# Kernel tuning notes

Hardware: AMD Instinct MI355X
Metric: run time of the kernel (lower is better)

## Reference

```python
import jax, jax.numpy as jnp
import numpy as np

D_MODEL = 1024
NUM_HEADS = 16
DEPTH = D_MODEL // NUM_HEADS


def setup_inputs() -> dict:
    key = jax.random.key(0)
    ks = jax.random.split(key, 9)
    B, S = 2, 2048
    s = 1.0 / np.sqrt(D_MODEL)
    inp = {
        "inputs": jax.random.normal(ks[0], (B, S, D_MODEL), dtype=jnp.float32),
        "wq": jax.random.normal(ks[1], (D_MODEL, D_MODEL), dtype=jnp.float32) * s,
        "bq": jnp.zeros((D_MODEL,), dtype=jnp.float32),
        "wk": jax.random.normal(ks[2], (D_MODEL, D_MODEL), dtype=jnp.float32) * s,
        "bk": jnp.zeros((D_MODEL,), dtype=jnp.float32),
        "wv": jax.random.normal(ks[3], (D_MODEL, D_MODEL), dtype=jnp.float32) * s,
        "bv": jnp.zeros((D_MODEL,), dtype=jnp.float32),
        "wo": jax.random.normal(ks[4], (D_MODEL, D_MODEL), dtype=jnp.float32) * s,
        "bo": jnp.zeros((D_MODEL,), dtype=jnp.float32),
    }
    return inp


def _split_heads(x, B):
    # [B, S, D] -> [B, H, S, depth]
    S = x.shape[1]
    return x.reshape(B, S, NUM_HEADS, DEPTH).transpose(0, 2, 1, 3)


def reference(inputs, wq, bq, wk, bk, wv, bv, wo, bo):
    B, S, _ = inputs.shape
    q = _split_heads(inputs @ wq + bq, B)  # [B,H,S,d]
    k = _split_heads(inputs @ wk + bk, B)
    v = _split_heads(inputs @ wv + bv, B)
    scale = 1.0 / jnp.sqrt(jnp.asarray(DEPTH, dtype=inputs.dtype))
    logits = jnp.einsum("bhqd,bhkd->bhqk", q, k) * scale  # [B,H,S,S]
    attn = jax.nn.softmax(logits, axis=-1)
    out = jnp.einsum("bhqk,bhkd->bhqd", attn, v)  # [B,H,S,d]
    out = out.transpose(0, 2, 1, 3).reshape(B, S, D_MODEL)
    return out @ wo + bo
```

## Files before the change

kernel.cpp:

```cpp
#include <hip/hip_runtime.h>
#include <math.h>

#define SEQ     2048
#define DM      1024
#define NH      16
#define DEPTH   64
#define MTOT    4096

typedef __attribute__((ext_vector_type(8))) _Float16 f16x8;
typedef __attribute__((ext_vector_type(2))) __fp16   fp16v2;
typedef __attribute__((ext_vector_type(4))) float    f32x4;
typedef __attribute__((ext_vector_type(2))) unsigned u32x2;

static __device__ inline unsigned pkh(float a, float b) {
    union { fp16v2 h; unsigned u; } c;
    c.h = __builtin_amdgcn_cvt_pkrtz(a, b);
    return c.u;
}

#define GLOBAL_AS(p) ((const __attribute__((address_space(1))) void*)(p))
#define LDS_AS(p)    ((__attribute__((address_space(3))) void*)(p))

#define K2  0.18033688011112043f
#define C2 -17.31234049066756f
#define EXP2(x) __builtin_amdgcn_exp2f(x)

#define DMA_SRC_C8(lane)  ((((lane) & 3) ^ (((lane) >> 3) & 3)) * 8)
#define FRAG_C8(lx,quad)  ((((quad) ^ (((lx) >> 1) & 3))) * 8)
#define DMA_SRC64(lane)   ((((lane) & 7) ^ (((lane) >> 3) & 7)) * 8)
#define FRAG64(lx,c)      ((((c) ^ ((lx) & 7))) * 8)

__global__ __launch_bounds__(256)
void prep(const float* __restrict__ X,
          const float* __restrict__ w0, const float* __restrict__ w1,
          const float* __restrict__ w2, const float* __restrict__ w3,
          short* __restrict__ Xb,
          short* __restrict__ o0, short* __restrict__ o1,
          short* __restrict__ o2, short* __restrict__ o3) {
    const int t = threadIdx.x;
    const int z = blockIdx.z;
    if (z >= 4) {
        int r0 = (z - 4) * 1024 + blockIdx.x * 64;
        int c0 = blockIdx.y * 64;
        #pragma unroll
        for (int i = 0; i < 4; i++) {
            int row = r0 + i * 16 + (t >> 4);
            int c4  = c0 + (t & 15) * 4;
            float4 v = *(const float4*)&X[(size_t)row * DM + c4];
            u32x2 o; o.x = pkh(v.x, v.y); o.y = pkh(v.z, v.w);
            *(u32x2*)&Xb[(size_t)row * DM + c4] = o;
        }
        return;
    }
    const float* W; short* O;
    switch (z) {
        case 0: W = w0; O = o0; break;
        case 1: W = w1; O = o1; break;
        case 2: W = w2; O = o2; break;
        default: W = w3; O = o3; break;
    }
    __shared__ float Tf[64][65];
    const int k0 = blockIdx.x * 64, n0 = blockIdx.y * 64;
    #pragma unroll
    for (int i = 0; i < 4; i++) {
        int row = i * 16 + (t >> 4);
        int c4  = (t & 15) * 4;
        float4 v = *(const float4*)&W[(size_t)(k0 + row) * DM + n0 + c4];
        Tf[row][c4 + 0] = v.x; Tf[row][c4 + 1] = v.y;
        Tf[row][c4 + 2] = v.z; Tf[row][c4 + 3] = v.w;
    }
    __syncthreads();
    #pragma unroll
    for (int i = 0; i < 4; i++) {
        int nrow = i * 16 + (t >> 4);
        int kc4  = (t & 15) * 4;
        u32x2 o;
        o.x = pkh(Tf[kc4 + 0][nrow], Tf[kc4 + 1][nrow]);
        o.y = pkh(Tf[kc4 + 2][nrow], Tf[kc4 + 3][nrow]);
        *(u32x2*)&O[(size_t)(n0 + nrow) * DM + k0 + kc4] = o;
    }
}

__global__ __launch_bounds__(256)
void gemm_qkv(const short* __restrict__ Xb,
              const short* __restrict__ Wqt, const short* __restrict__ Wkt,
              const short* __restrict__ Wvt,
              const float* __restrict__ bq, const float* __restrict__ bk,
              const float* __restrict__ bv,
              short* __restrict__ Qw, short* __restrict__ Kw,
              short* __restrict__ Vtw) {
    const int z = blockIdx.z;
    const short* A; const short* B; const float* bias;
    if (z == 0)      { A = Xb;  B = Wqt; bias = bq; }
    else if (z == 1) { A = Xb;  B = Wkt; bias = bk; }
    else             { A = Wvt; B = Xb;  bias = bv; }
    const int bx = blockIdx.x;
    int m0, n0;
    if (z < 2) { n0 = (bx & 7) * 128; m0 = (bx >> 3) * 128; }
    else       { m0 = (bx & 7) * 128; n0 = (bx >> 3) * 128; }

    __shared__ short As[128 * 64];
    __shared__ short Bs[128 * 64];
    const int t = threadIdx.x, lane = t & 63, w = t >> 6;
    const int lx = lane & 15, quad = lane >> 4;
    const int wm = (w & 1) * 64, wn = (w >> 1) * 64;
    const int r8 = lane >> 3;
    const int cs = DMA_SRC64(lane);

    f32x4 acc[4][4];
    #pragma unroll
    for (int i = 0; i < 4; i++)
        #pragma unroll
        for (int j = 0; j < 4; j++)
            acc[i][j] = (f32x4){0.f, 0.f, 0.f, 0.f};

    for (int k0 = 0; k0 < DM; k0 += 64) {
        #pragma unroll
        for (int j = 0; j < 4; j++) {
            int rb = w * 32 + j * 8;
            __builtin_amdgcn_global_load_lds(
                GLOBAL_AS(A + (size_t)(m0 + rb + r8) * DM + k0 + cs),
                LDS_AS(As + rb * 64), 16, 0, 0);
            __builtin_amdgcn_global_load_lds(
                GLOBAL_AS(B + (size_t)(n0 + rb + r8) * DM + k0 + cs),
                LDS_AS(Bs + rb * 64), 16, 0, 0);
        }
        __syncthreads();

        #pragma unroll
        for (int ks = 0; ks < 2; ks++) {
            const int fo = FRAG64(lx, ks * 4 + quad);
            f16x8 af[4], bfr[4];
            #pragma unroll
            for (int mt = 0; mt < 4; mt++)
                af[mt] = *(f16x8*)&As[(wm + mt * 16 + lx) * 64 + fo];
            #pragma unroll
            for (int nt = 0; nt < 4; nt++)
                bfr[nt] = *(f16x8*)&Bs[(wn + nt * 16 + lx) * 64 + fo];
            #pragma unroll
            for (int mt = 0; mt < 4; mt++)
                #pragma unroll
                for (int nt = 0; nt < 4; nt++)
                    acc[mt][nt] = __builtin_amdgcn_mfma_f32_16x16x32_f16(
                        af[mt], bfr[nt], acc[mt][nt], 0, 0, 0);
        }
        __syncthreads();
    }

    if (z < 2) {
        short* Cp = (z == 0) ? Qw : Kw;
        float bi[4];
        #pragma unroll
        for (int nt = 0; nt < 4; nt++) bi[nt] = bias[n0 + wn + nt * 16 + lx];
        #pragma unroll
        for (int mt = 0; mt < 4; mt++) {
            #pragma unroll
            for (int reg = 0; reg < 4; reg++) {
                int row = m0 + wm + mt * 16 + quad * 4 + reg;
                u32x2 o;
                o.x = pkh(acc[mt][0][reg] + bi[0], acc[mt][1][reg] + bi[1]);
                o.y = pkh(acc[mt][2][reg] + bi[2], acc[mt][3][reg] + bi[3]);
                *(u32x2*)&Cp[(size_t)row * DM + n0 + wn + 4 * lx] = o;
            }
        }
    } else {
        int colbase = n0 + wn;
        int bsel    = colbase >> 11;
        int kb      = (colbase & 2047) & ~63;
        short* Vbh  = Vtw + (size_t)bsel * ((size_t)NH * DEPTH * SEQ);
        #pragma unroll
        for (int mt = 0; mt < 4; mt++) {
            #pragma unroll
            for (int reg = 0; reg < 4; reg++) {
                int row = m0 + wm + mt * 16 + quad * 4 + reg;
                float bb = bias[row];
                u32x2 o;
                o.x = pkh(acc[mt][0][reg] + bb, acc[mt][1][reg] + bb);
                o.y = pkh(acc[mt][2][reg] + bb, acc[mt][3][reg] + bb);
                *(u32x2*)&Vbh[(size_t)row * SEQ + kb + 4 * lx] = o;
            }
        }
    }
}

__global__ __launch_bounds__(256)
void gemm_out(const short* __restrict__ A, const short* __restrict__ B,
              const float* __restrict__ bias, float* __restrict__ C) {
    __shared__ short As[128 * 64];
    __shared__ short Bs[64 * 64];
    const int t = threadIdx.x, lane = t & 63, w = t >> 6;
    const int lx = lane & 15, quad = lane >> 4;
    const int n0 = blockIdx.x * 64, m0 = blockIdx.y * 128;
    const int wm = (w & 1) * 64, wn = (w >> 1) * 32;
    const int r8 = lane >> 3;
    const int cs = DMA_SRC64(lane);

    f32x4 acc[4][2];
    #pragma unroll
    for (int i = 0; i < 4; i++)
        #pragma unroll
        for (int j = 0; j < 2; j++)
            acc[i][j] = (f32x4){0.f, 0.f, 0.f, 0.f};

    for (int k0 = 0; k0 < DM; k0 += 64) {
        #pragma unroll
        for (int j = 0; j < 4; j++) {
            int rb = w * 32 + j * 8;
            __builtin_amdgcn_global_load_lds(
                GLOBAL_AS(A + (size_t)(m0 + rb + r8) * DM + k0 + cs),
                LDS_AS(As + rb * 64), 16, 0, 0);
        }
        #pragma unroll
        for (int j = 0; j < 2; j++) {
            int rb = w * 16 + j * 8;
            __builtin_amdgcn_global_load_lds(
                GLOBAL_AS(B + (size_t)(n0 + rb + r8) * DM + k0 + cs),
                LDS_AS(Bs + rb * 64), 16, 0, 0);
        }
        __syncthreads();

        #pragma unroll
        for (int ks = 0; ks < 2; ks++) {
            const int fo = FRAG64(lx, ks * 4 + quad);
            f16x8 af[4], bfr[2];
            #pragma unroll
            for (int mt = 0; mt < 4; mt++)
                af[mt] = *(f16x8*)&As[(wm + mt * 16 + lx) * 64 + fo];
            #pragma unroll
            for (int nt = 0; nt < 2; nt++)
                bfr[nt] = *(f16x8*)&Bs[(wn + nt * 16 + lx) * 64 + fo];
            #pragma unroll
            for (int mt = 0; mt < 4; mt++)
                #pragma unroll
                for (int nt = 0; nt < 2; nt++)
                    acc[mt][nt] = __builtin_amdgcn_mfma_f32_16x16x32_f16(
                        af[mt], bfr[nt], acc[mt][nt], 0, 0, 0);
        }
        __syncthreads();
    }

    #pragma unroll
    for (int mt = 0; mt < 4; mt++)
        #pragma unroll
        for (int nt = 0; nt < 2; nt++)
            #pragma unroll
            for (int reg = 0; reg < 4; reg++) {
                int row = m0 + wm + mt * 16 + quad * 4 + reg;
                int col = n0 + wn + nt * 16 + lx;
                C[(size_t)row * DM + col] = acc[mt][nt][reg] + bias[col];
            }
}

__global__ __launch_bounds__(256)
void flash_mfma(const short* __restrict__ Q, const short* __restrict__ K,
                const short* __restrict__ Vt, short* __restrict__ O) {
    __shared__ short Ks[2][2][64 * 32];
    __shared__ short Vs[2][2][64 * 32];
    __shared__ short Ps[128 * 72];

    const int t = threadIdx.x, lane = t & 63, w = t >> 6;
    const int lx = lane & 15, quad = lane >> 4;
    const int h = blockIdx.y, bb = blockIdx.z;
    const int q0 = blockIdx.x * 128;
    const int r4 = lane >> 2;
    const int cs  = DMA_SRC_C8(lane);
    const int fa  = FRAG_C8(lx, quad);

    f16x8 qa[2][2];
    #pragma unroll
    for (int mt = 0; mt < 2; mt++)
        #pragma unroll
        for (int ks = 0; ks < 2; ks++)
            qa[mt][ks] = *(const f16x8*)&Q[(size_t)(bb * SEQ + q0 + w * 32 + mt * 16 + lx) * DM
                                           + h * DEPTH + ks * 32 + quad * 8];

    f32x4 of[2][4];
    float l_acc[2][4];
    #pragma unroll
    for (int mt = 0; mt < 2; mt++) {
        #pragma unroll
        for (int dt = 0; dt < 4; dt++) of[mt][dt] = (f32x4){0.f, 0.f, 0.f, 0.f};
        #pragma unroll
        for (int reg = 0; reg < 4; reg++) l_acc[mt][reg] = 0.f;
    }

    const short* Kb = K  + (size_t)bb * SEQ * DM + h * DEPTH;
    const short* Vb = Vt + (size_t)(bb * NH + h) * DEPTH * SEQ;

    auto stage = [&](int kt, int sb) {
        const int kbase = kt * 64;
        const short* kg = Kb + (size_t)(kbase + w * 16 + r4) * DM;
        __builtin_amdgcn_global_load_lds(GLOBAL_AS(kg + cs),
                                         LDS_AS(&Ks[sb][0][w * 16 * 32]), 16, 0, 0);
        __builtin_amdgcn_global_load_lds(GLOBAL_AS(kg + 32 + cs),
                                         LDS_AS(&Ks[sb][1][w * 16 * 32]), 16, 0, 0);
        const short* vg = Vb + (size_t)(w * 16 + r4) * SEQ + kbase;
        __builtin_amdgcn_global_load_lds(GLOBAL_AS(vg + cs),
                                         LDS_AS(&Vs[sb][0][w * 16 * 32]), 16, 0, 0);
        __builtin_amdgcn_global_load_lds(GLOBAL_AS(vg + 32 + cs),
                                         LDS_AS(&Vs[sb][1][w * 16 * 32]), 16, 0, 0);
    };

    stage(0, 0);
    __syncthreads();

    int buf = 0;
    for (int kt = 0; kt < SEQ / 64; kt++) {
        if (kt + 1 < SEQ / 64) stage(kt + 1, buf ^ 1);

        f32x4 s[2][4];
        #pragma unroll
        for (int mt = 0; mt < 2; mt++)
            #pragma unroll
            for (int nt = 0; nt < 4; nt++)
                s[mt][nt] = (f32x4){0.f, 0.f, 0.f, 0.f};
        #pragma unroll
        for (int ks = 0; ks < 2; ks++) {
            f16x8 kb[4];
            #pragma unroll
            for (int nt = 0; nt < 4; nt++)
                kb[nt] = *(f16x8*)&Ks[buf][ks][(nt * 16 + lx) * 32 + fa];
            __builtin_amdgcn_s_setprio(1);
            #pragma unroll
            for (int mt = 0; mt < 2; mt++)
                #pragma unroll
                for (int nt = 0; nt < 4; nt++)
                    s[mt][nt] = __builtin_amdgcn_mfma_f32_16x16x32_f16(
                        qa[mt][ks], kb[nt], s[mt][nt], 0, 0, 0);
            __builtin_amdgcn_s_setprio(0);
        }

        #pragma unroll
        for (int mt = 0; mt < 2; mt++) {
            #pragma unroll
            for (int reg = 0; reg < 4; reg++) {
                float p0 = EXP2(fmaf(s[mt][0][reg], K2, C2));
                float p1 = EXP2(fmaf(s[mt][1][reg], K2, C2));
                float p2 = EXP2(fmaf(s[mt][2][reg], K2, C2));
                float p3 = EXP2(fmaf(s[mt][3][reg], K2, C2));
                l_acc[mt][reg] += (p0 + p1) + (p2 + p3);
                int rowoff = (w * 32 + mt * 16 + quad * 4 + reg) * 72;
                u32x2 pk; pk.x = pkh(p0, p1); pk.y = pkh(p2, p3);
                *(u32x2*)&Ps[rowoff + 4 * lx] = pk;
            }
        }

        #pragma unroll
        for (int ks = 0; ks < 2; ks++) {
            f16x8 vb[4], pa[2];
            #pragma unroll
            for (int dt = 0; dt < 4; dt++)
                vb[dt] = *(f16x8*)&Vs[buf][ks][(dt * 16 + lx) * 32 + fa];
            #pragma unroll
            for (int mt = 0; mt < 2; mt++)
                pa[mt] = *(f16x8*)&Ps[(w * 32 + mt * 16 + lx) * 72 + ks * 32 + quad * 8];
            __builtin_amdgcn_s_setprio(1);
            #pragma unroll
            for (int mt = 0; mt < 2; mt++)
                #pragma unroll
                for (int dt = 0; dt < 4; dt++)
                    of[mt][dt] = __builtin_amdgcn_mfma_f32_16x16x32_f16(
                        pa[mt], vb[dt], of[mt][dt], 0, 0, 0);
            __builtin_amdgcn_s_setprio(0);
        }

        __syncthreads();
        buf ^= 1;
    }

    _Float16* Oh = (_Float16*)O;
    #pragma unroll
    for (int mt = 0; mt < 2; mt++) {
        #pragma unroll
        for (int reg = 0; reg < 4; reg++) {
            float l = l_acc[mt][reg];
            l += __shfl_xor(l, 1);
            l += __shfl_xor(l, 2);
            l += __shfl_xor(l, 4);
            l += __shfl_xor(l, 8);
            float inv = 1.0f / l;
            size_t row = (size_t)bb * SEQ + q0 + w * 32 + mt * 16 + quad * 4 + reg;
            #pragma unroll
            for (int dt = 0; dt < 4; dt++)
                Oh[row * DM + h * DEPTH + dt * 16 + lx] = (_Float16)(of[mt][dt][reg] * inv);
        }
    }
}

extern "C" void kernel_launch(void* const* d_in, const int* in_sizes, int n_in,
                              void* d_out, int out_size, void* d_ws, size_t ws_size,
                              hipStream_t stream) {
    const float* X  = (const float*)d_in[0];
    const float* wq = (const float*)d_in[1];
    const float* bq = (const float*)d_in[2];
    const float* wk = (const float*)d_in[3];
    const float* bk = (const float*)d_in[4];
    const float* wv = (const float*)d_in[5];
    const float* bv = (const float*)d_in[6];
    const float* wo = (const float*)d_in[7];
    const float* bo = (const float*)d_in[8];
    float* out = (float*)d_out;

    short* Xb  = (short*)d_ws;
    short* Wqt = Xb  + (size_t)MTOT * DM;
    short* Wkt = Wqt + (size_t)DM * DM;
    short* Wvt = Wkt + (size_t)DM * DM;
    short* Wot = Wvt + (size_t)DM * DM;
    short* Qw  = Wot + (size_t)DM * DM;
    short* Kw  = Qw  + (size_t)MTOT * DM;
    short* Vtw = Kw  + (size_t)MTOT * DM;
    short* AO  = Vtw + (size_t)MTOT * DM;

    hipLaunchKernelGGL(prep, dim3(16, 16, 8), dim3(256), 0, stream,
                       X, wq, wk, wv, wo, Xb, Wqt, Wkt, Wvt, Wot);

    hipLaunchKernelGGL(gemm_qkv, dim3(256, 1, 3), dim3(256), 0, stream,
                       Xb, Wqt, Wkt, Wvt, bq, bk, bv, Qw, Kw, Vtw);

    hipLaunchKernelGGL(flash_mfma, dim3(SEQ / 128, NH, 2), dim3(256), 0, stream,
                       Qw, Kw, Vtw, AO);

    hipLaunchKernelGGL(gemm_out, dim3(16, 32), dim3(256), 0, stream,
                       AO, Wot, bo, out);
}
```

Measured before the change: 206.5 us.

## Keep softmax probabilities in registers via transposed QK^T MFMA and permuted V layout

Computes S^T by swapping MFMA operands (K as A, Q as B), so each lane holds scores along the key dimension in a layout that can be packed directly into the A-operand fragment of the PV MFMA. The Ps shared-memory round trip for probabilities is removed. To match this, the V projection epilogue now writes V^T with a permuted key ordering within each 64-column block. The row-sum reduction changes from per-row shuffles inside the loop's output stage to cross-quad shuffles plus a broadcast at the end. This drops LDS writes and reads for P and some LDS footprint, but it depends on the permuted V layout matching the register fragment order exactly.

```diff
diff --git a/kernel.cpp b/kernel.cpp
--- a/kernel.cpp
+++ b/kernel.cpp
@@ -166,18 +166,19 @@
     } else {
         int colbase = n0 + wn;
         int bsel    = colbase >> 11;
-        int kb      = (colbase & 2047) & ~63;
+        int kb      = colbase & 2047;
         short* Vbh  = Vtw + (size_t)bsel * ((size_t)NH * DEPTH * SEQ);
+        int so = ((lx >> 2) * 8) + ((lx & 3) * 2);
         #pragma unroll
         for (int mt = 0; mt < 4; mt++) {
             #pragma unroll
             for (int reg = 0; reg < 4; reg++) {
                 int row = m0 + wm + mt * 16 + quad * 4 + reg;
                 float bb = bias[row];
-                u32x2 o;
-                o.x = pkh(acc[mt][0][reg] + bb, acc[mt][1][reg] + bb);
-                o.y = pkh(acc[mt][2][reg] + bb, acc[mt][3][reg] + bb);
-                *(u32x2*)&Vbh[(size_t)row * SEQ + kb + 4 * lx] = o;
+                unsigned w01 = pkh(acc[mt][0][reg] + bb, acc[mt][1][reg] + bb);
+                unsigned w23 = pkh(acc[mt][2][reg] + bb, acc[mt][3][reg] + bb);
+                *(unsigned*)&Vbh[(size_t)row * SEQ + kb + so]      = w01;
+                *(unsigned*)&Vbh[(size_t)row * SEQ + kb + so + 32] = w23;
             }
         }
     }
@@ -256,7 +257,6 @@
                 const short* __restrict__ Vt, short* __restrict__ O) {
     __shared__ short Ks[2][2][64 * 32];
     __shared__ short Vs[2][2][64 * 32];
-    __shared__ short Ps[128 * 72];
 
     const int t = threadIdx.x, lane = t & 63, w = t >> 6;
     const int lx = lane & 15, quad = lane >> 4;
@@ -275,13 +275,12 @@
                                            + h * DEPTH + ks * 32 + quad * 8];
 
     f32x4 of[2][4];
-    float l_acc[2][4];
+    float l_acc[2];
     #pragma unroll
     for (int mt = 0; mt < 2; mt++) {
         #pragma unroll
         for (int dt = 0; dt < 4; dt++) of[mt][dt] = (f32x4){0.f, 0.f, 0.f, 0.f};
-        #pragma unroll
-        for (int reg = 0; reg < 4; reg++) l_acc[mt][reg] = 0.f;
+        l_acc[mt] = 0.f;
     }
 
     const short* Kb = K  + (size_t)bb * SEQ * DM + h * DEPTH;
@@ -308,12 +307,12 @@
     for (int kt = 0; kt < SEQ / 64; kt++) {
         if (kt + 1 < SEQ / 64) stage(kt + 1, buf ^ 1);
 
-        f32x4 s[2][4];
-        #pragma unroll
-        for (int mt = 0; mt < 2; mt++)
-            #pragma unroll
-            for (int nt = 0; nt < 4; nt++)
-                s[mt][nt] = (f32x4){0.f, 0.f, 0.f, 0.f};
+        f32x4 st[4][2];
+        #pragma unroll
+        for (int nt = 0; nt < 4; nt++)
+            #pragma unroll
+            for (int mt = 0; mt < 2; mt++)
+                st[nt][mt] = (f32x4){0.f, 0.f, 0.f, 0.f};
         #pragma unroll
         for (int ks = 0; ks < 2; ks++) {
             f16x8 kb[4];
@@ -322,45 +321,46 @@
                 kb[nt] = *(f16x8*)&Ks[buf][ks][(nt * 16 + lx) * 32 + fa];
             __builtin_amdgcn_s_setprio(1);
             #pragma unroll
-            for (int mt = 0; mt < 2; mt++)
+            for (int nt = 0; nt < 4; nt++)
                 #pragma unroll
-                for (int nt = 0; nt < 4; nt++)
-                    s[mt][nt] = __builtin_amdgcn_mfma_f32_16x16x32_f16(
-                        qa[mt][ks], kb[nt], s[mt][nt], 0, 0, 0);
+                for (int mt = 0; mt < 2; mt++)
+                    st[nt][mt] = __builtin_amdgcn_mfma_f32_16x16x32_f16(
+                        kb[nt], qa[mt][ks], st[nt][mt], 0, 0, 0);
             __builtin_amdgcn_s_setprio(0);
         }
 
+        f16x8 pa[2][2];
         #pragma unroll
         for (int mt = 0; mt < 2; mt++) {
-            #pragma unroll
-            for (int reg = 0; reg < 4; reg++) {
-                float p0 = EXP2(fmaf(s[mt][0][reg], K2, C2));
-                float p1 = EXP2(fmaf(s[mt][1][reg], K2, C2));
-                float p2 = EXP2(fmaf(s[mt][2][reg], K2, C2));
-                float p3 = EXP2(fmaf(s[mt][3][reg], K2, C2));
-                l_acc[mt][reg] += (p0 + p1) + (p2 + p3);
-                int rowoff = (w * 32 + mt * 16 + quad * 4 + reg) * 72;
-                u32x2 pk; pk.x = pkh(p0, p1); pk.y = pkh(p2, p3);
-                *(u32x2*)&Ps[rowoff + 4 * lx] = pk;
+            float lsum = 0.f;
+            #pragma unroll
+            for (int ks = 0; ks < 2; ks++) {
+                union { f16x8 v; unsigned u[4]; } pu;
+                #pragma unroll
+                for (int wd = 0; wd < 4; wd++) {
+                    float pe = EXP2(fmaf(st[2 * ks + 0][mt][wd], K2, C2));
+                    float po = EXP2(fmaf(st[2 * ks + 1][mt][wd], K2, C2));
+                    lsum += pe + po;
+                    pu.u[wd] = pkh(pe, po);
+                }
+                pa[mt][ks] = pu.v;
             }
+            l_acc[mt] += lsum;
         }
 
         #pragma unroll
         for (int ks = 0; ks < 2; ks++) {
-            f16x8 vb[4], pa[2];
+            f16x8 vb[4];
             #pragma unroll
             for (int dt = 0; dt < 4; dt++)
                 vb[dt] = *(f16x8*)&Vs[buf][ks][(dt * 16 + lx) * 32 + fa];
-            #pragma unroll
-            for (int mt = 0; mt < 2; mt++)
-                pa[mt] = *(f16x8*)&Ps[(w * 32 + mt * 16 + lx) * 72 + ks * 32 + quad * 8];
             __builtin_amdgcn_s_setprio(1);
             #pragma unroll
             for (int mt = 0; mt < 2; mt++)
                 #pragma unroll
                 for (int dt = 0; dt < 4; dt++)
                     of[mt][dt] = __builtin_amdgcn_mfma_f32_16x16x32_f16(
-                        pa[mt], vb[dt], of[mt][dt], 0, 0, 0);
+                        pa[mt][ks], vb[dt], of[mt][dt], 0, 0, 0);
             __builtin_amdgcn_s_setprio(0);
         }
 
@@ -371,14 +371,13 @@
     _Float16* Oh = (_Float16*)O;
     #pragma unroll
     for (int mt = 0; mt < 2; mt++) {
+        float l = l_acc[mt];
+        l += __shfl_xor(l, 16);
+        l += __shfl_xor(l, 32);
         #pragma unroll
         for (int reg = 0; reg < 4; reg++) {
-            float l = l_acc[mt][reg];
-            l += __shfl_xor(l, 1);
-            l += __shfl_xor(l, 2);
-            l += __shfl_xor(l, 4);
-            l += __shfl_xor(l, 8);
-            float inv = 1.0f / l;
+            float lrow = __shfl(l, quad * 4 + reg, 64);
+            float inv  = 1.0f / lrow;
             size_t row = (size_t)bb * SEQ + q0 + w * 32 + mt * 16 + quad * 4 + reg;
             #pragma unroll
             for (int dt = 0; dt < 4; dt++)
```

Result: no change. 205.2 us (-0.6%).
